# Kernel optimization log

Hardware: AMD Instinct MI355X
Metric: run time of the kernel (lower is better)

Reference implementation:

```python
import jax, jax.numpy as jnp
import numpy as np

BATCH = 2048
DIM = 256
HID = 512
NCLS = 10
TPTS = 8
SUBSTEPS = 4  # fixed dopri5 substeps per time interval


def setup_inputs() -> dict:
    key = jax.random.key(0)
    ks = jax.random.split(key, 8)
    s1 = 1.0 / np.sqrt(DIM)
    s2 = 1.0 / np.sqrt(HID)
    return {
        "x0": jax.random.normal(ks[0], (BATCH, DIM), jnp.float32),
        "t": jnp.arange(TPTS, dtype=jnp.float32) / (TPTS - 1),
        "W1": jax.random.normal(ks[1], (DIM, HID), jnp.float32) * s1,
        "b1": jnp.zeros((HID,), jnp.float32),
        "W2": jax.random.normal(ks[2], (HID, DIM), jnp.float32) * s2,
        "b2": jnp.zeros((DIM,), jnp.float32),
        "Wc1": jax.random.normal(ks[3], (DIM, 64), jnp.float32) * s1,
        "bc1": jnp.zeros((64,), jnp.float32),
        "Wc2": jax.random.normal(ks[4], (64, NCLS), jnp.float32) * 0.125,
        "bc2": jnp.zeros((NCLS,), jnp.float32),
    }


def reference(x0, t, W1, b1, W2, b2, Wc1, bc1, Wc2, bc2):
    # ODE function: dy/dt = f(t, y) = tanh(y @ W1 + b1) @ W2 + b2
    def f(ti, y):
        return jnp.tanh(y @ W1 + b1) @ W2 + b2

    # Fixed substep grid: SUBSTEPS equal dopri5 steps per [t_i, t_{i+1}] interval.
    dt_int = (t[1:] - t[:-1]) / SUBSTEPS                      # [TPTS-1]
    frac = jnp.arange(SUBSTEPS, dtype=t.dtype)
    starts = (t[:-1, None] + dt_int[:, None] * frac).reshape(-1)  # [(TPTS-1)*SUBSTEPS]
    dts = jnp.repeat(dt_int, SUBSTEPS)

    def dopri5_step(y, td):
        ti, dt = td
        k1 = f(ti, y)
        k2 = f(ti + dt * (1.0 / 5), y + dt * (1.0 / 5) * k1)
        k3 = f(ti + dt * (3.0 / 10), y + dt * (3.0 / 40 * k1 + 9.0 / 40 * k2))
        k4 = f(ti + dt * (4.0 / 5), y + dt * (44.0 / 45 * k1 - 56.0 / 15 * k2 + 32.0 / 9 * k3))
        k5 = f(ti + dt * (8.0 / 9), y + dt * (19372.0 / 6561 * k1 - 25360.0 / 2187 * k2
                                              + 64448.0 / 6561 * k3 - 212.0 / 729 * k4))
        k6 = f(ti + dt, y + dt * (9017.0 / 3168 * k1 - 355.0 / 33 * k2 + 46732.0 / 5247 * k3
                                  + 49.0 / 176 * k4 - 5103.0 / 18656 * k5))
        # 5th-order solution weights (b7 = 0, FSAL)
        y_next = y + dt * (35.0 / 384 * k1 + 500.0 / 1113 * k3 + 125.0 / 192 * k4
                           - 2187.0 / 6784 * k5 + 11.0 / 84 * k6)
        return y_next, None

    yT, _ = jax.lax.scan(dopri5_step, x0, (starts, dts))  # final state at t[-1]

    # classifier head (Dropout is identity in eval mode)
    h = jax.nn.relu(yT @ Wc1 + bc1)
    logits = h @ Wc2 + bc2
    return logits
```

## Files before the change

kernel.cpp:

```cpp
#include <hip/hip_runtime.h>

typedef _Float16 f16;
typedef _Float16 f16x8 __attribute__((ext_vector_type(8)));
typedef float f32x4 __attribute__((ext_vector_type(4)));

#define DIM 256
#define HID 512

#define WSO_W1  0
#define WSO_W2  131072
#define WSO_WC1 262144
#define WSO_WC2 278528
#define PACK_TOTAL 279552

#define LDS_W1   0
#define LDS_YST  131072
#define LDS_HB   139264
#define SMEM_BYTES 155648

#define MFMA(a, b, c) __builtin_amdgcn_mfma_f32_16x16x32_f16(a, b, c, 0, 0, 0)

__global__ void pack_weights(const float* __restrict__ W1, const float* __restrict__ W2,
                             const float* __restrict__ Wc1, const float* __restrict__ Wc2,
                             f16* __restrict__ ws) {
    int gid = blockIdx.x * 256 + threadIdx.x;
    if (gid >= PACK_TOTAL) return;
    if (gid < WSO_W2) {
        int g = gid;
        int j = g & 7, lane = (g >> 3) & 63, fi = g >> 9;
        int kt = fi >> 5, nt = fi & 31;
        int k = kt * 32 + ((lane >> 4) << 3) + j;
        int n = (nt << 4) + (lane & 15);
        ws[WSO_W1 + g] = (f16)W1[k * HID + n];
    } else if (gid < WSO_WC1) {
        int g = gid - WSO_W2;
        int j = g & 7, lane = (g >> 3) & 63, fi = g >> 9;
        int kt = fi >> 4, nt = fi & 15;
        int k = kt * 32 + ((lane >> 4) << 3) + j;
        int n = (nt << 4) + (lane & 15);
        ws[WSO_W2 + g] = (f16)W2[k * DIM + n];
    } else if (gid < WSO_WC2) {
        int g = gid - WSO_WC1;
        int j = g & 7, lane = (g >> 3) & 63, fi = g >> 9;
        int kt = fi >> 2, nt = fi & 3;
        int k = kt * 32 + ((lane >> 4) << 3) + j;
        int n = (nt << 4) + (lane & 15);
        ws[WSO_WC1 + g] = (f16)Wc1[k * 64 + n];
    } else {
        int g = gid - WSO_WC2;
        int j = g & 7, lane = (g >> 3) & 63, kt = g >> 9;
        int k = kt * 32 + ((lane >> 4) << 3) + j;
        int n = lane & 15;
        ws[WSO_WC2 + g] = (n < 10) ? (f16)Wc2[k * 10 + n] : (f16)0.0f;
    }
}

__device__ __forceinline__ float tanh_fast(float x) {
    float e = __expf(2.0f * x);
    return 1.0f - 2.0f * __builtin_amdgcn_rcpf(e + 1.0f);
}

template <class FIN, class FOUT>
__device__ __forceinline__ void feval(FIN yin, FOUT kout,
        const f16* __restrict__ ws, const f16* w1lds, f16* yst, f16* hbuf,
        const f16x8 (&w1r)[4][3], const f16x8 (&w2r)[2][8],
        int lane, int w, const float b1c[4], const float b2c[2]) {
    const int cn   = lane & 15;
    const int rlo  = (lane >> 4) << 2;
    const int koff = (lane >> 4) << 3;

#define LDW1(KT, Q) (*(const f16x8*)(ws + WSO_W1 + ((((KT) * 32 + 4 * w + (Q)) << 9) + lane * 8)))
#define LDW2(KT, T) (*(const f16x8*)(ws + WSO_W2 + ((((KT) * 16 + 2 * w + (T)) << 9) + lane * 8)))

    f16x8 w1s[4];
    #pragma unroll
    for (int q = 0; q < 4; ++q) w1s[q] = LDW1(3, q);
    f16x8 w2s[4][2];
    #pragma unroll
    for (int st = 0; st < 4; ++st) {
        w2s[st][0] = LDW2(8 + st, 0);
        w2s[st][1] = LDW2(8 + st, 1);
    }

    #pragma unroll
    for (int t = 0; t < 2; ++t)
        #pragma unroll
        for (int i = 0; i < 4; ++i) {
            int row = rlo + i;
            int col = w * 32 + t * 16 + cn;
            int idx = ((row << 8) + col) ^ ((row & 7) << 3);
            yst[idx] = (f16)yin(t, i);
        }
    __syncthreads();

    f32x4 acc[4];
    #pragma unroll
    for (int q = 0; q < 4; ++q) acc[q] = (f32x4){0.f, 0.f, 0.f, 0.f};
    const int kord[8] = {0, 1, 2, 4, 5, 6, 7, 3};
    #pragma unroll
    for (int s = 0; s < 8; ++s) {
        const int kt = kord[s];
        int aidx = ((cn << 8) + kt * 32 + koff) ^ ((cn & 7) << 3);
        f16x8 af = *(const f16x8*)(yst + aidx);
        #pragma unroll
        for (int q = 0; q < 4; ++q) {
            f16x8 wf;
            if (kt < 3)       wf = w1r[q][kt];
            else if (kt == 3) wf = w1s[q];
            else              wf = *(const f16x8*)(w1lds + (((kt - 4) * 32 + 4 * w + q) << 9) + lane * 8);
            acc[q] = MFMA(af, wf, acc[q]);
        }
    }
    #pragma unroll
    for (int q = 0; q < 4; ++q) {
        int hcol = ((4 * w + q) << 4) + cn;
        #pragma unroll
        for (int i = 0; i < 4; ++i) {
            float th = tanh_fast(acc[q][i] + b1c[q]);
            int row = rlo + i;
            int idx = ((row << 9) + hcol) ^ ((row & 7) << 3);
            hbuf[idx] = (f16)th;
        }
    }
    __syncthreads();

    f32x4 acc2[2];
    acc2[0] = (f32x4){0.f, 0.f, 0.f, 0.f};
    acc2[1] = (f32x4){0.f, 0.f, 0.f, 0.f};

#define M2STEP(KT, B0, B1) { \
        int aidx = ((cn << 9) + (KT) * 32 + koff) ^ ((cn & 7) << 3); \
        f16x8 af = *(const f16x8*)(hbuf + aidx); \
        acc2[0] = MFMA(af, B0, acc2[0]); \
        acc2[1] = MFMA(af, B1, acc2[1]); }

    #pragma unroll
    for (int st = 0; st < 4; ++st) {
        M2STEP(8 + st, w2s[st][0], w2s[st][1]);
        w2s[st][0] = LDW2(12 + st, 0);
        w2s[st][1] = LDW2(12 + st, 1);
    }
    #pragma unroll
    for (int kt = 0; kt < 4; ++kt) M2STEP(kt, w2r[0][kt], w2r[1][kt]);
    #pragma unroll
    for (int st = 0; st < 4; ++st) M2STEP(12 + st, w2s[st][0], w2s[st][1]);
    #pragma unroll
    for (int kt = 4; kt < 8; ++kt) M2STEP(kt, w2r[0][kt], w2r[1][kt]);
#undef M2STEP
#undef LDW1
#undef LDW2

    #pragma unroll
    for (int t = 0; t < 2; ++t)
        #pragma unroll
        for (int i = 0; i < 4; ++i)
            kout(t, i, acc2[t][i] + b2c[t]);
}

__launch_bounds__(512, 2)
__global__ void ode_main(const float* __restrict__ x0, const float* __restrict__ tg,
                         const float* __restrict__ b1, const float* __restrict__ b2,
                         const float* __restrict__ bc1, const float* __restrict__ bc2,
                         const f16* __restrict__ ws, float* __restrict__ out) {
    extern __shared__ char smem[];
    f16* w1lds = (f16*)(smem + LDS_W1);
    f16* yst   = (f16*)(smem + LDS_YST);
    f16* hbuf  = (f16*)(smem + LDS_HB);

    const int tid  = threadIdx.x;
    const int lane = tid & 63;
    const int w    = tid >> 6;
    const int r0   = blockIdx.x * 16;
    const int cn   = lane & 15;
    const int rlo  = (lane >> 4) << 2;

    #pragma unroll
    for (int u = 0; u < 16; ++u) {
        int e = (u * 512 + tid) * 8;
        *(f16x8*)(w1lds + e) = *(const f16x8*)(ws + WSO_W1 + 65536 + e);
    }

    f16x8 w1r[4][3];
    #pragma unroll
    for (int q = 0; q < 4; ++q)
        #pragma unroll
        for (int kt = 0; kt < 3; ++kt)
            w1r[q][kt] = *(const f16x8*)(ws + WSO_W1 + (((kt * 32 + 4 * w + q) << 9) + lane * 8));

    f16x8 w2r[2][8];
    #pragma unroll
    for (int t = 0; t < 2; ++t)
        #pragma unroll
        for (int kt = 0; kt < 8; ++kt)
            w2r[t][kt] = *(const f16x8*)(ws + WSO_W2 + (((kt * 16 + 2 * w + t) << 9) + lane * 8));

    float b1c[4], b2c[2];
    #pragma unroll
    for (int q = 0; q < 4; ++q) b1c[q] = b1[((4 * w + q) << 4) + cn];
    #pragma unroll
    for (int t = 0; t < 2; ++t) b2c[t] = b2[((2 * w + t) << 4) + cn];

    float y[2][4];
    #pragma unroll
    for (int t = 0; t < 2; ++t)
        #pragma unroll
        for (int i = 0; i < 4; ++i)
            y[t][i] = x0[(r0 + rlo + i) * DIM + w * 32 + t * 16 + cn];

    __syncthreads();

    float k1[2][4], k2[2][4], k3[2][4], k4[2][4], k5[2][4];
    float dt = 0.f;

    for (int s = 0; s < 28; ++s) {
        if ((s & 3) == 0) { int iv = s >> 2; dt = (tg[iv + 1] - tg[iv]) * 0.25f; }

        feval([&](int t, int i) { return y[t][i]; },
              [&](int t, int i, float v) { k1[t][i] = v; },
              ws, w1lds, yst, hbuf, w1r, w2r, lane, w, b1c, b2c);
        feval([&](int t, int i) { return y[t][i] + dt * 0.2f * k1[t][i]; },
              [&](int t, int i, float v) { k2[t][i] = v; },
              ws, w1lds, yst, hbuf, w1r, w2r, lane, w, b1c, b2c);
        feval([&](int t, int i) { return y[t][i] + dt * (0.075f * k1[t][i] + 0.225f * k2[t][i]); },
              [&](int t, int i, float v) { k3[t][i] = v; },
              ws, w1lds, yst, hbuf, w1r, w2r, lane, w, b1c, b2c);
        feval([&](int t, int i) { return y[t][i] + dt * ((44.f/45.f) * k1[t][i] + (-56.f/15.f) * k2[t][i]
                                                        + (32.f/9.f) * k3[t][i]); },
              [&](int t, int i, float v) { k4[t][i] = v; },
              ws, w1lds, yst, hbuf, w1r, w2r, lane, w, b1c, b2c);
        feval([&](int t, int i) { return y[t][i] + dt * ((19372.f/6561.f) * k1[t][i] + (-25360.f/2187.f) * k2[t][i]
                                                        + (64448.f/6561.f) * k3[t][i] + (-212.f/729.f) * k4[t][i]); },
              [&](int t, int i, float v) { k5[t][i] = v; },
              ws, w1lds, yst, hbuf, w1r, w2r, lane, w, b1c, b2c);
        feval([&](int t, int i) { return y[t][i] + dt * ((9017.f/3168.f) * k1[t][i] + (-355.f/33.f) * k2[t][i]
                                                        + (46732.f/5247.f) * k3[t][i] + (49.f/176.f) * k4[t][i]
                                                        + (-5103.f/18656.f) * k5[t][i]); },
              [&](int t, int i, float v) {
                  y[t][i] += dt * ((35.f/384.f)    * k1[t][i] + (500.f/1113.f)  * k3[t][i]
                                 + (125.f/192.f)   * k4[t][i] + (-2187.f/6784.f) * k5[t][i]
                                 + (11.f/84.f)     * v);
              },
              ws, w1lds, yst, hbuf, w1r, w2r, lane, w, b1c, b2c);
    }

    #pragma unroll
    for (int t = 0; t < 2; ++t)
        #pragma unroll
        for (int i = 0; i < 4; ++i) {
            int row = rlo + i;
            int col = w * 32 + t * 16 + cn;
            int idx = ((row << 8) + col) ^ ((row & 7) << 3);
            yst[idx] = (f16)y[t][i];
        }
    __syncthreads();

    if (w < 4) {
        const int koff = (lane >> 4) << 3;
        f32x4 ha = (f32x4){0.f, 0.f, 0.f, 0.f};
        #pragma unroll
        for (int kt = 0; kt < 8; ++kt) {
            int aidx = ((cn << 8) + kt * 32 + koff) ^ ((cn & 7) << 3);
            f16x8 af = *(const f16x8*)(yst + aidx);
            f16x8 wf = *(const f16x8*)(ws + WSO_WC1 + (((kt * 4 + w) << 9) + lane * 8));
            ha = MFMA(af, wf, ha);
        }
        float bb = bc1[(w << 4) + cn];
        #pragma unroll
        for (int i = 0; i < 4; ++i) {
            float v = fmaxf(ha[i] + bb, 0.f);
            int row = rlo + i;
            int idx = ((row << 6) + (w << 4) + cn) ^ ((row & 7) << 3);
            hbuf[idx] = (f16)v;
        }
    }
    __syncthreads();

    if (w == 0) {
        const int koff = (lane >> 4) << 3;
        f32x4 acc = (f32x4){0.f, 0.f, 0.f, 0.f};
        #pragma unroll
        for (int kt = 0; kt < 2; ++kt) {
            int aidx = ((cn << 6) + kt * 32 + koff) ^ ((cn & 7) << 3);
            f16x8 af = *(const f16x8*)(hbuf + aidx);
            f16x8 wf = *(const f16x8*)(ws + WSO_WC2 + ((kt << 9) + lane * 8));
            acc = MFMA(af, wf, acc);
        }
        if (cn < 10) {
            float bb = bc2[cn];
            #pragma unroll
            for (int i = 0; i < 4; ++i)
                out[(r0 + rlo + i) * 10 + cn] = acc[i] + bb;
        }
    }
}

extern "C" void kernel_launch(void* const* d_in, const int* in_sizes, int n_in,
                              void* d_out, int out_size, void* d_ws, size_t ws_size,
                              hipStream_t stream) {
    const float* x0  = (const float*)d_in[0];
    const float* tg  = (const float*)d_in[1];
    const float* W1  = (const float*)d_in[2];
    const float* b1  = (const float*)d_in[3];
    const float* W2  = (const float*)d_in[4];
    const float* b2  = (const float*)d_in[5];
    const float* Wc1 = (const float*)d_in[6];
    const float* bc1 = (const float*)d_in[7];
    const float* Wc2 = (const float*)d_in[8];
    const float* bc2 = (const float*)d_in[9];
    f16* ws = (f16*)d_ws;
    float* out = (float*)d_out;

    hipFuncSetAttribute((const void*)ode_main,
                        hipFuncAttributeMaxDynamicSharedMemorySize, SMEM_BYTES);

    pack_weights<<<(PACK_TOTAL + 255) / 256, 256, 0, stream>>>(W1, W2, Wc1, Wc2, ws);
    ode_main<<<128, 512, SMEM_BYTES, stream>>>(x0, tg, b1, b2, bc1, bc2, ws, out);
}
```

Baseline: 1.676 ms.

## Stream all weights from global via rotating register buffers, pack RK stages as fp16

Drops the register-resident W1 and W2 fragments, which were held across every evaluation. The W1 k-tiles not in LDS and all 16 W2 k-tiles now stream from global/L2 through a small rotating prefetch buffer interleaved with the MFMAs. The RK stage vectors k1..k5 are stored as packed fp16 instead of fp32, and launch_bounds drops the min-2-blocks hint. The aim is to cut register pressure, but it adds global weight traffic on every function evaluation and loses precision in the stage values.

```diff
diff --git a/kernel.cpp b/kernel.cpp
--- a/kernel.cpp
+++ b/kernel.cpp
@@ -1,6 +1,7 @@
 #include <hip/hip_runtime.h>
 
 typedef _Float16 f16;
+typedef _Float16 f16x2 __attribute__((ext_vector_type(2)));
 typedef _Float16 f16x8 __attribute__((ext_vector_type(8)));
 typedef float f32x4 __attribute__((ext_vector_type(4)));
 
@@ -63,7 +64,6 @@
 template <class FIN, class FOUT>
 __device__ __forceinline__ void feval(FIN yin, FOUT kout,
         const f16* __restrict__ ws, const f16* w1lds, f16* yst, f16* hbuf,
-        const f16x8 (&w1r)[4][3], const f16x8 (&w2r)[2][8],
         int lane, int w, const float b1c[4], const float b2c[2]) {
     const int cn   = lane & 15;
     const int rlo  = (lane >> 4) << 2;
@@ -71,16 +71,6 @@
 
 #define LDW1(KT, Q) (*(const f16x8*)(ws + WSO_W1 + ((((KT) * 32 + 4 * w + (Q)) << 9) + lane * 8)))
 #define LDW2(KT, T) (*(const f16x8*)(ws + WSO_W2 + ((((KT) * 16 + 2 * w + (T)) << 9) + lane * 8)))
-
-    f16x8 w1s[4];
-    #pragma unroll
-    for (int q = 0; q < 4; ++q) w1s[q] = LDW1(3, q);
-    f16x8 w2s[4][2];
-    #pragma unroll
-    for (int st = 0; st < 4; ++st) {
-        w2s[st][0] = LDW2(8 + st, 0);
-        w2s[st][1] = LDW2(8 + st, 1);
-    }
 
     #pragma unroll
     for (int t = 0; t < 2; ++t)
@@ -93,24 +83,42 @@
         }
     __syncthreads();
 
+    f16x8 w1s[4];
+    #pragma unroll
+    for (int q = 0; q < 4; ++q) w1s[q] = LDW1(0, q);
+
     f32x4 acc[4];
     #pragma unroll
     for (int q = 0; q < 4; ++q) acc[q] = (f32x4){0.f, 0.f, 0.f, 0.f};
-    const int kord[8] = {0, 1, 2, 4, 5, 6, 7, 3};
-    #pragma unroll
-    for (int s = 0; s < 8; ++s) {
-        const int kt = kord[s];
-        int aidx = ((cn << 8) + kt * 32 + koff) ^ ((cn & 7) << 3);
-        f16x8 af = *(const f16x8*)(yst + aidx);
-        #pragma unroll
-        for (int q = 0; q < 4; ++q) {
-            f16x8 wf;
-            if (kt < 3)       wf = w1r[q][kt];
-            else if (kt == 3) wf = w1s[q];
-            else              wf = *(const f16x8*)(w1lds + (((kt - 4) * 32 + 4 * w + q) << 9) + lane * 8);
-            acc[q] = MFMA(af, wf, acc[q]);
-        }
-    }
+
+#define M1_LDS(KT) { \
+        int aidx = ((cn << 8) + (KT) * 32 + koff) ^ ((cn & 7) << 3); \
+        f16x8 af = *(const f16x8*)(yst + aidx); \
+        _Pragma("unroll") \
+        for (int q = 0; q < 4; ++q) { \
+            f16x8 wf = *(const f16x8*)(w1lds + ((((KT) - 4) * 32 + 4 * w + q) << 9) + lane * 8); \
+            acc[q] = MFMA(af, wf, acc[q]); } }
+#define M1_STR(KT, RKT, DOREF) { \
+        int aidx = ((cn << 8) + (KT) * 32 + koff) ^ ((cn & 7) << 3); \
+        f16x8 af = *(const f16x8*)(yst + aidx); \
+        f16x8 t0 = w1s[0], t1 = w1s[1], t2 = w1s[2], t3 = w1s[3]; \
+        if (DOREF) { \
+            w1s[0] = LDW1(RKT, 0); w1s[1] = LDW1(RKT, 1); \
+            w1s[2] = LDW1(RKT, 2); w1s[3] = LDW1(RKT, 3); } \
+        acc[0] = MFMA(af, t0, acc[0]); acc[1] = MFMA(af, t1, acc[1]); \
+        acc[2] = MFMA(af, t2, acc[2]); acc[3] = MFMA(af, t3, acc[3]); }
+
+    M1_LDS(4)
+    M1_LDS(5)
+    M1_STR(0, 1, 1)
+    M1_LDS(6)
+    M1_STR(1, 2, 1)
+    M1_LDS(7)
+    M1_STR(2, 3, 1)
+    M1_STR(3, 3, 0)
+#undef M1_LDS
+#undef M1_STR
+
     #pragma unroll
     for (int q = 0; q < 4; ++q) {
         int hcol = ((4 * w + q) << 4) + cn;
@@ -124,29 +132,32 @@
     }
     __syncthreads();
 
+    f16x8 w2s[4][2];
+    #pragma unroll
+    for (int st = 0; st < 4; ++st) {
+        w2s[st][0] = LDW2(st, 0);
+        w2s[st][1] = LDW2(st, 1);
+    }
+
     f32x4 acc2[2];
     acc2[0] = (f32x4){0.f, 0.f, 0.f, 0.f};
     acc2[1] = (f32x4){0.f, 0.f, 0.f, 0.f};
 
-#define M2STEP(KT, B0, B1) { \
+#define M2(KT) { \
         int aidx = ((cn << 9) + (KT) * 32 + koff) ^ ((cn & 7) << 3); \
         f16x8 af = *(const f16x8*)(hbuf + aidx); \
-        acc2[0] = MFMA(af, B0, acc2[0]); \
-        acc2[1] = MFMA(af, B1, acc2[1]); }
-
-    #pragma unroll
-    for (int st = 0; st < 4; ++st) {
-        M2STEP(8 + st, w2s[st][0], w2s[st][1]);
-        w2s[st][0] = LDW2(12 + st, 0);
-        w2s[st][1] = LDW2(12 + st, 1);
-    }
-    #pragma unroll
-    for (int kt = 0; kt < 4; ++kt) M2STEP(kt, w2r[0][kt], w2r[1][kt]);
-    #pragma unroll
-    for (int st = 0; st < 4; ++st) M2STEP(12 + st, w2s[st][0], w2s[st][1]);
-    #pragma unroll
-    for (int kt = 4; kt < 8; ++kt) M2STEP(kt, w2r[0][kt], w2r[1][kt]);
-#undef M2STEP
+        f16x8 b0 = w2s[(KT) & 3][0], b1v = w2s[(KT) & 3][1]; \
+        if ((KT) < 12) { \
+            w2s[(KT) & 3][0] = LDW2((KT) + 4, 0); \
+            w2s[(KT) & 3][1] = LDW2((KT) + 4, 1); } \
+        acc2[0] = MFMA(af, b0, acc2[0]); \
+        acc2[1] = MFMA(af, b1v, acc2[1]); }
+
+    M2(0)  M2(1)  M2(2)  M2(3)
+    M2(4)  M2(5)  M2(6)  M2(7)
+    M2(8)  M2(9)  M2(10) M2(11)
+    M2(12) M2(13) M2(14) M2(15)
+#undef M2
 #undef LDW1
 #undef LDW2
 
@@ -157,7 +168,7 @@
             kout(t, i, acc2[t][i] + b2c[t]);
 }
 
-__launch_bounds__(512, 2)
+__launch_bounds__(512)
 __global__ void ode_main(const float* __restrict__ x0, const float* __restrict__ tg,
                          const float* __restrict__ b1, const float* __restrict__ b2,
                          const float* __restrict__ bc1, const float* __restrict__ bc2,
@@ -180,20 +191,6 @@
         *(f16x8*)(w1lds + e) = *(const f16x8*)(ws + WSO_W1 + 65536 + e);
     }
 
-    f16x8 w1r[4][3];
-    #pragma unroll
-    for (int q = 0; q < 4; ++q)
-        #pragma unroll
-        for (int kt = 0; kt < 3; ++kt)
-            w1r[q][kt] = *(const f16x8*)(ws + WSO_W1 + (((kt * 32 + 4 * w + q) << 9) + lane * 8));
-
-    f16x8 w2r[2][8];
-    #pragma unroll
-    for (int t = 0; t < 2; ++t)
-        #pragma unroll
-        for (int kt = 0; kt < 8; ++kt)
-            w2r[t][kt] = *(const f16x8*)(ws + WSO_W2 + (((kt * 16 + 2 * w + t) << 9) + lane * 8));
-
     float b1c[4], b2c[2];
     #pragma unroll
     for (int q = 0; q < 4; ++q) b1c[q] = b1[((4 * w + q) << 4) + cn];
@@ -209,39 +206,44 @@
 
     __syncthreads();
 
-    float k1[2][4], k2[2][4], k3[2][4], k4[2][4], k5[2][4];
+    f16x2 k1p[2][2], k2p[2][2], k3p[2][2], k4p[2][2], k5p[2][2];
     float dt = 0.f;
+
+#define KGET(P, t, i) ((float)P[t][(i) >> 1][(i) & 1])
+#define KPUT(P, t, i, v) P[t][(i) >> 1][(i) & 1] = (f16)(v)
 
     for (int s = 0; s < 28; ++s) {
         if ((s & 3) == 0) { int iv = s >> 2; dt = (tg[iv + 1] - tg[iv]) * 0.25f; }
 
         feval([&](int t, int i) { return y[t][i]; },
-              [&](int t, int i, float v) { k1[t][i] = v; },
-              ws, w1lds, yst, hbuf, w1r, w2r, lane, w, b1c, b2c);
-        feval([&](int t, int i) { return y[t][i] + dt * 0.2f * k1[t][i]; },
-              [&](int t, int i, float v) { k2[t][i] = v; },
-              ws, w1lds, yst, hbuf, w1r, w2r, lane, w, b1c, b2c);
-        feval([&](int t, int i) { return y[t][i] + dt * (0.075f * k1[t][i] + 0.225f * k2[t][i]); },
-              [&](int t, int i, float v) { k3[t][i] = v; },
-              ws, w1lds, yst, hbuf, w1r, w2r, lane, w, b1c, b2c);
-        feval([&](int t, int i) { return y[t][i] + dt * ((44.f/45.f) * k1[t][i] + (-56.f/15.f) * k2[t][i]
-                                                        + (32.f/9.f) * k3[t][i]); },
-              [&](int t, int i, float v) { k4[t][i] = v; },
-              ws, w1lds, yst, hbuf, w1r, w2r, lane, w, b1c, b2c);
-        feval([&](int t, int i) { return y[t][i] + dt * ((19372.f/6561.f) * k1[t][i] + (-25360.f/2187.f) * k2[t][i]
-                                                        + (64448.f/6561.f) * k3[t][i] + (-212.f/729.f) * k4[t][i]); },
-              [&](int t, int i, float v) { k5[t][i] = v; },
-              ws, w1lds, yst, hbuf, w1r, w2r, lane, w, b1c, b2c);
-        feval([&](int t, int i) { return y[t][i] + dt * ((9017.f/3168.f) * k1[t][i] + (-355.f/33.f) * k2[t][i]
-                                                        + (46732.f/5247.f) * k3[t][i] + (49.f/176.f) * k4[t][i]
-                                                        + (-5103.f/18656.f) * k5[t][i]); },
+              [&](int t, int i, float v) { KPUT(k1p, t, i, v); },
+              ws, w1lds, yst, hbuf, lane, w, b1c, b2c);
+        feval([&](int t, int i) { return y[t][i] + dt * 0.2f * KGET(k1p, t, i); },
+              [&](int t, int i, float v) { KPUT(k2p, t, i, v); },
+              ws, w1lds, yst, hbuf, lane, w, b1c, b2c);
+        feval([&](int t, int i) { return y[t][i] + dt * (0.075f * KGET(k1p, t, i) + 0.225f * KGET(k2p, t, i)); },
+              [&](int t, int i, float v) { KPUT(k3p, t, i, v); },
+              ws, w1lds, yst, hbuf, lane, w, b1c, b2c);
+        feval([&](int t, int i) { return y[t][i] + dt * ((44.f/45.f) * KGET(k1p, t, i) + (-56.f/15.f) * KGET(k2p, t, i)
+                                                        + (32.f/9.f) * KGET(k3p, t, i)); },
+              [&](int t, int i, float v) { KPUT(k4p, t, i, v); },
+              ws, w1lds, yst, hbuf, lane, w, b1c, b2c);
+        feval([&](int t, int i) { return y[t][i] + dt * ((19372.f/6561.f) * KGET(k1p, t, i) + (-25360.f/2187.f) * KGET(k2p, t, i)
+                                                        + (64448.f/6561.f) * KGET(k3p, t, i) + (-212.f/729.f) * KGET(k4p, t, i)); },
+              [&](int t, int i, float v) { KPUT(k5p, t, i, v); },
+              ws, w1lds, yst, hbuf, lane, w, b1c, b2c);
+        feval([&](int t, int i) { return y[t][i] + dt * ((9017.f/3168.f) * KGET(k1p, t, i) + (-355.f/33.f) * KGET(k2p, t, i)
+                                                        + (46732.f/5247.f) * KGET(k3p, t, i) + (49.f/176.f) * KGET(k4p, t, i)
+                                                        + (-5103.f/18656.f) * KGET(k5p, t, i)); },
               [&](int t, int i, float v) {
-                  y[t][i] += dt * ((35.f/384.f)    * k1[t][i] + (500.f/1113.f)  * k3[t][i]
-                                 + (125.f/192.f)   * k4[t][i] + (-2187.f/6784.f) * k5[t][i]
+                  y[t][i] += dt * ((35.f/384.f)    * KGET(k1p, t, i) + (500.f/1113.f)  * KGET(k3p, t, i)
+                                 + (125.f/192.f)   * KGET(k4p, t, i) + (-2187.f/6784.f) * KGET(k5p, t, i)
                                  + (11.f/84.f)     * v);
               },
-              ws, w1lds, yst, hbuf, w1r, w2r, lane, w, b1c, b2c);
-    }
+              ws, w1lds, yst, hbuf, lane, w, b1c, b2c);
+    }
+#undef KGET
+#undef KPUT
 
     #pragma unroll
     for (int t = 0; t < 2; ++t)
```

After: 1.630 ms. -2.7%, faster.
